# Kernel tuning notes

Measured on AMD Instinct MI355X. Metric: run time of the kernel, lower is better.

Reference implementation:

```python
import jax, jax.numpy as jnp
import numpy as np

N, E, D = 20000, 320000, 256
H, C = 8, 32  # heads, per-head channels (out_channels // heads)


def setup_inputs() -> dict:
    key = jax.random.key(0)
    ks = jax.random.split(key, 12)
    s = 1.0 / np.sqrt(D)
    return {
        "x": jax.random.normal(ks[0], (N, D), jnp.float32),
        "edge_index": jax.random.randint(ks[1], (2, E), 0, N, jnp.int64),
        "edge_attr": jax.random.normal(ks[2], (E, D), jnp.float32),
        "Wq": jax.random.normal(ks[3], (D, H * C), jnp.float32) * s,
        "bq": jnp.zeros((H * C,), jnp.float32),
        "Wk": jax.random.normal(ks[4], (D, H * C), jnp.float32) * s,
        "bk": jnp.zeros((H * C,), jnp.float32),
        "Wv": jax.random.normal(ks[5], (D, H * C), jnp.float32) * s,
        "bv": jnp.zeros((H * C,), jnp.float32),
        "We": jax.random.normal(ks[6], (D, H * C), jnp.float32) * s,  # lin_edge, no bias
        "Ws": jax.random.normal(ks[7], (D, H * C), jnp.float32) * s,  # lin_skip (root weight)
        "bs": jnp.zeros((H * C,), jnp.float32),
    }


def reference(x, edge_index, edge_attr, Wq, bq, Wk, bk, Wv, bv, We, Ws, bs):
    n = x.shape[0]
    src, dst = edge_index[0], edge_index[1]  # j (source), i (target)
    q = (x @ Wq + bq).reshape(n, H, C)
    k = (x @ Wk + bk).reshape(n, H, C)
    v = (x @ Wv + bv).reshape(n, H, C)
    e = (edge_attr @ We).reshape(-1, H, C)  # (E, H, C)

    kj = k[src] + e                      # key of source node + edge embedding
    alpha = jnp.einsum('ehc,ehc->eh', q[dst], kj) / jnp.sqrt(jnp.float32(C))
    # numerically-stable segment softmax over destination neighborhoods
    amax = jax.ops.segment_max(alpha, dst, num_segments=n)      # (N, H)
    ea = jnp.exp(alpha - amax[dst])                             # (E, H)
    denom = jax.ops.segment_sum(ea, dst, num_segments=n)        # (N, H)
    alpha = ea / (denom[dst] + 1e-16)

    msg = (v[src] + e) * alpha[:, :, None]                      # (E, H, C)
    out = jax.ops.segment_sum(msg, dst, num_segments=n)         # (N, H, C)
    out = out.reshape(n, H * C) + (x @ Ws + bs)                 # concat heads + skip
    return out
```

## Files before the change

### kernel.cpp

```cpp
#include <hip/hip_runtime.h>
#include <hip/hip_fp16.h>

#define N_NODES 20000
#define N_EDGES 320000
#define DIM 256

typedef _Float16 f16;
typedef unsigned int u32;
typedef f16 f16x8 __attribute__((ext_vector_type(8)));
typedef f16 f16x4 __attribute__((ext_vector_type(4)));
typedef float f32x4 __attribute__((ext_vector_type(4)));

#define GLL16(gsrc, ldst) __builtin_amdgcn_global_load_lds( \
    (const u32 __attribute__((address_space(1)))*)(gsrc),   \
    (u32 __attribute__((address_space(3)))*)(ldst), 16, 0, 0)

__global__ void prep_all(const float* __restrict__ Wq, const float* __restrict__ Wk,
                         const float* __restrict__ Wv, const float* __restrict__ Ws,
                         const float* __restrict__ We,
                         const float* __restrict__ bq, const float* __restrict__ bk,
                         const float* __restrict__ bv, const float* __restrict__ bs,
                         f16* __restrict__ wtbase, float* __restrict__ biasAll,
                         int* __restrict__ deg) {
    if (blockIdx.x < 1280) {
        int gid = blockIdx.x * 256 + threadIdx.x;
        int w = gid >> 16;
        int idx = gid & 65535;
        int k = idx >> 8, n = idx & 255;
        const float* W = (w == 0) ? Wq : (w == 1) ? Wk : (w == 2) ? Wv : (w == 3) ? Ws : We;
        wtbase[w * 65536 + n * 256 + k] = (f16)W[k * 256 + n];
    } else if (blockIdx.x < 1284) {
        int i = (blockIdx.x - 1280) * 256 + threadIdx.x;
        int y = i >> 8, col = i & 255;
        const float* b = (y == 0) ? bq : (y == 1) ? bk : (y == 2) ? bv : bs;
        biasAll[i] = b[col];
    } else {
        int i = (blockIdx.x - 1284) * 256 + threadIdx.x;
        if (i < N_NODES) deg[i] = 0;
    }
}

template<int EDGE>
__global__ __launch_bounds__(512, 4) void gemm_v4(
    const float* __restrict__ A, const f16* __restrict__ WTbase,
    const float* __restrict__ biasAll, const int* __restrict__ eids,
    f16* __restrict__ outF16, float* __restrict__ outF32, int M)
{
    __shared__ __align__(16) char lds[65536];
    const int tid = threadIdx.x;
    const int wave = tid >> 6, lane = tid & 63;
    const int l16 = lane & 15, lg = lane >> 4;
    const int y = blockIdx.y;
    const int outSel  = EDGE ? 4 : (y >> 1);
    const int colHalf = EDGE ? y : (y & 1);
    const f16* __restrict__ WT = WTbase + outSel * 65536 + colHalf * 128 * 256;
    const int rowBase = blockIdx.x * 128 + wave * 16;

    const int slot = rowBase + l16;
    int arow;
    if (EDGE) arow = eids[slot];
    else      arow = (slot < M) ? slot : M - 1;
    const float* ap = A + (size_t)arow * DIM;
    f32x4 lo[8], hi[8];
#pragma unroll
    for (int ks = 0; ks < 8; ++ks) {
        lo[ks] = *(const f32x4*)(ap + ks * 32 + lg * 8);
        hi[ks] = *(const f32x4*)(ap + ks * 32 + lg * 8 + 4);
    }

    {
        const int p = lane & 31;
#pragma unroll
        for (int r = 0; r < 8; ++r) {
            const int nrel = wave * 16 + r * 2 + (lane >> 5);
            const f16* src = WT + nrel * 256 + (p ^ (nrel & 31)) * 8;
            GLL16(src, &lds[(wave * 16 + r * 2) * 512]);
        }
    }

    f16x8 afr[8];
#pragma unroll
    for (int ks = 0; ks < 8; ++ks) {
#pragma unroll
        for (int j = 0; j < 4; ++j) {
            afr[ks][j]     = (f16)lo[ks][j];
            afr[ks][4 + j] = (f16)hi[ks][j];
        }
    }

    f32x4 acc[8];
#pragma unroll
    for (int c = 0; c < 8; ++c) acc[c] = (f32x4){0.f, 0.f, 0.f, 0.f};

    __syncthreads();

#pragma unroll
    for (int ks = 0; ks < 8; ++ks) {
#pragma unroll
        for (int ct = 0; ct < 8; ++ct) {
            const int nrel = ct * 16 + l16;
            f16x8 b = *(const f16x8*)(lds + nrel * 512 + (((ks * 4 + lg) ^ (nrel & 31)) * 16));
            acc[ct] = __builtin_amdgcn_mfma_f32_16x16x32_f16(afr[ks], b, acc[ct], 0, 0, 0);
        }
    }

#pragma unroll
    for (int ct = 0; ct < 8; ++ct) {
        const int col = colHalf * 128 + ct * 16 + l16;
        const float bv = EDGE ? 0.f : biasAll[outSel * 256 + col];
#pragma unroll
        for (int i = 0; i < 4; ++i) {
            const int row = rowBase + lg * 4 + i;
            if (EDGE || row < M) {
                const float val = acc[ct][i] + bv;
                if (EDGE) {
                    outF16[(size_t)row * 256 + col] = (f16)val;
                } else if (outSel < 3) {
                    (outF16 + (size_t)outSel * N_NODES * 256)[(size_t)row * 256 + col] = (f16)val;
                } else {
                    outF32[(size_t)row * 256 + col] = val;
                }
            }
        }
    }
}

__global__ void count_deg(const int* __restrict__ dst, int* __restrict__ deg) {
    int e = blockIdx.x * blockDim.x + threadIdx.x;
    if (e < N_EDGES) atomicAdd(&deg[dst[e]], 1);
}

__global__ __launch_bounds__(1024) void scan_deg(const int* __restrict__ deg,
                                                 int* __restrict__ rowptr,
                                                 int* __restrict__ cursor) {
    __shared__ int part[1024];
    const int t = threadIdx.x;
    const int CH = (N_NODES + 1023) / 1024;
    const int base = t * CH;
    int s = 0;
    for (int i = 0; i < CH; ++i) { int n = base + i; if (n < N_NODES) s += deg[n]; }
    part[t] = s;
    __syncthreads();
    for (int off = 1; off < 1024; off <<= 1) {
        int v = (t >= off) ? part[t - off] : 0;
        __syncthreads();
        part[t] += v;
        __syncthreads();
    }
    int run = (t == 0) ? 0 : part[t - 1];
    for (int i = 0; i < CH; ++i) {
        int n = base + i;
        if (n < N_NODES) { int dn = deg[n]; rowptr[n] = run; cursor[n] = run; run += dn; }
    }
    if (t == 1023) rowptr[N_NODES] = part[1023];
}

__global__ void scatter_edges(const int* __restrict__ src, const int* __restrict__ dst,
                              int* __restrict__ cursor,
                              int* __restrict__ eids, int* __restrict__ srcs) {
    int e = blockIdx.x * blockDim.x + threadIdx.x;
    if (e < N_EDGES) {
        int p = atomicAdd(&cursor[dst[e]], 1);
        eids[p] = e;
        srcs[p] = src[e];
    }
}

__global__ __launch_bounds__(256) void aggregate(
    const f16* __restrict__ qf, const f16* __restrict__ kf, const f16* __restrict__ vf,
    const f16* __restrict__ ef, const int* __restrict__ srcs,
    const int* __restrict__ rowptr, float* __restrict__ out)
{
    const int wave = threadIdx.x >> 6;
    const int lane = threadIdx.x & 63;
    const int node = blockIdx.x * 4 + wave;
    if (node >= N_NODES) return;
    const int c0 = lane * 4;

    f32x4 qv;
    {
        f16x4 qh = *(const f16x4*)(qf + (size_t)node * 256 + c0);
        qv = (f32x4){(float)qh[0], (float)qh[1], (float)qh[2], (float)qh[3]};
    }
    float acc0 = 0.f, acc1 = 0.f, acc2 = 0.f, acc3 = 0.f, den = 0.f;
    const int beg = rowptr[node], end = rowptr[node + 1];

#define BODY(ii) {                                                              \
        const int src = srcs[ii];                                               \
        f16x4 eh = *(const f16x4*)(ef + (size_t)(ii) * 256 + c0);               \
        f16x4 kh = *(const f16x4*)(kf + (size_t)src * 256 + c0);                \
        f16x4 vh = *(const f16x4*)(vf + (size_t)src * 256 + c0);                \
        const float e0 = (float)eh[0], e1 = (float)eh[1];                       \
        const float e2 = (float)eh[2], e3 = (float)eh[3];                       \
        float d = qv[0] * ((float)kh[0] + e0) + qv[1] * ((float)kh[1] + e1)     \
                + qv[2] * ((float)kh[2] + e2) + qv[3] * ((float)kh[3] + e3);    \
        d += __shfl_xor(d, 1);                                                  \
        d += __shfl_xor(d, 2);                                                  \
        d += __shfl_xor(d, 4);                                                  \
        const float w_ = __expf(d * 0.1767766952966369f);                       \
        den += w_;                                                              \
        acc0 += w_ * ((float)vh[0] + e0);                                       \
        acc1 += w_ * ((float)vh[1] + e1);                                       \
        acc2 += w_ * ((float)vh[2] + e2);                                       \
        acc3 += w_ * ((float)vh[3] + e3);                                       \
    }

    int idx = beg;
    for (; idx + 1 < end; idx += 2) { BODY(idx); BODY(idx + 1); }
    if (idx < end) BODY(idx);
#undef BODY

    const float inv = 1.0f / (den + 1e-16f);
    const size_t ob = (size_t)node * 256 + c0;
    f32x4 o = *(f32x4*)(out + ob);
    o[0] += acc0 * inv; o[1] += acc1 * inv; o[2] += acc2 * inv; o[3] += acc3 * inv;
    *(f32x4*)(out + ob) = o;
}

extern "C" void kernel_launch(void* const* d_in, const int* in_sizes, int n_in,
                              void* d_out, int out_size, void* d_ws, size_t ws_size,
                              hipStream_t stream) {
    const float* x   = (const float*)d_in[0];
    const int*   ei  = (const int*)d_in[1];
    const float* ea  = (const float*)d_in[2];
    const float* Wq  = (const float*)d_in[3];
    const float* bq  = (const float*)d_in[4];
    const float* Wk  = (const float*)d_in[5];
    const float* bk  = (const float*)d_in[6];
    const float* Wv  = (const float*)d_in[7];
    const float* bv  = (const float*)d_in[8];
    const float* We  = (const float*)d_in[9];
    const float* Ws  = (const float*)d_in[10];
    const float* bs  = (const float*)d_in[11];
    float* out = (float*)d_out;

    const int* srcArr = ei;
    const int* dstArr = ei + N_EDGES;

    char* w = (char*)d_ws;
    size_t off = 0;
    f16* wtbase = (f16*)(w + off); off += 5 * 65536 * 2;
    f16* qf = (f16*)(w + off); off += (size_t)N_NODES * 256 * 2;
    f16* kf = (f16*)(w + off); off += (size_t)N_NODES * 256 * 2;
    f16* vf = (f16*)(w + off); off += (size_t)N_NODES * 256 * 2;
    f16* ef = (f16*)(w + off); off += (size_t)N_EDGES * 256 * 2;
    int* deg    = (int*)(w + off); off += 80016;
    int* rowptr = (int*)(w + off); off += 80016;
    int* cursor = (int*)(w + off); off += 80016;
    int* eids   = (int*)(w + off); off += (size_t)N_EDGES * 4;
    int* srcs   = (int*)(w + off); off += (size_t)N_EDGES * 4;
    float* biasAll = (float*)(w + off); off += 4 * 256 * 4;
    (void)ws_size; (void)n_in; (void)in_sizes; (void)out_size;

    prep_all<<<1284 + (N_NODES + 255) / 256, 256, 0, stream>>>(
        Wq, Wk, Wv, Ws, We, bq, bk, bv, bs, wtbase, biasAll, deg);

    count_deg<<<(N_EDGES + 255) / 256, 256, 0, stream>>>(dstArr, deg);
    scan_deg<<<1, 1024, 0, stream>>>(deg, rowptr, cursor);
    scatter_edges<<<(N_EDGES + 255) / 256, 256, 0, stream>>>(srcArr, dstArr, cursor, eids, srcs);

    dim3 gnode((N_NODES + 127) / 128, 8);
    gemm_v4<0><<<gnode, 512, 0, stream>>>(x, wtbase, biasAll, nullptr, qf, out, N_NODES);
    dim3 gedge(N_EDGES / 128, 2);
    gemm_v4<1><<<gedge, 512, 0, stream>>>(ea, wtbase, nullptr, eids, ef, nullptr, N_EDGES);

    aggregate<<<N_NODES / 4, 256, 0, stream>>>(qf, kf, vf, ef, srcs, rowptr, out);
}
```

Baseline: 389.6 us.

## Make GEMMs persistent with software-pipelined A loads, scatter edge outputs, unroll aggregate

Both projection GEMMs become persistent kernels with a fixed grid of 512 blocks. Each block loads its weight slice into LDS once and loops over row tiles, prefetching the next half-tile of A while the MFMAs run. The edge GEMM now reads edge_attr contiguously and scatters results into CSR order through a slot-of-edge map, instead of gathering rows through eids. The aggregate loop is unrolled by 4 with all loads issued up front to raise memory-level parallelism, at the cost of more registers and scattered f16 writes.

```diff
diff --git a/kernel.cpp b/kernel.cpp
--- a/kernel.cpp
+++ b/kernel.cpp
@@ -41,32 +41,26 @@
 }
 
 template<int EDGE>
-__global__ __launch_bounds__(512, 4) void gemm_v4(
+__global__ __launch_bounds__(512, 4) void gemm_v5(
     const float* __restrict__ A, const f16* __restrict__ WTbase,
-    const float* __restrict__ biasAll, const int* __restrict__ eids,
-    f16* __restrict__ outF16, float* __restrict__ outF32, int M)
+    const float* __restrict__ biasAll, const int* __restrict__ slotOf,
+    f16* __restrict__ outF16, float* __restrict__ outF32)
 {
     __shared__ __align__(16) char lds[65536];
     const int tid = threadIdx.x;
     const int wave = tid >> 6, lane = tid & 63;
     const int l16 = lane & 15, lg = lane >> 4;
-    const int y = blockIdx.y;
-    const int outSel  = EDGE ? 4 : (y >> 1);
-    const int colHalf = EDGE ? y : (y & 1);
-    const f16* __restrict__ WT = WTbase + outSel * 65536 + colHalf * 128 * 256;
-    const int rowBase = blockIdx.x * 128 + wave * 16;
-
-    const int slot = rowBase + l16;
-    int arow;
-    if (EDGE) arow = eids[slot];
-    else      arow = (slot < M) ? slot : M - 1;
-    const float* ap = A + (size_t)arow * DIM;
-    f32x4 lo[8], hi[8];
-#pragma unroll
-    for (int ks = 0; ks < 8; ++ks) {
-        lo[ks] = *(const f32x4*)(ap + ks * 32 + lg * 8);
-        hi[ks] = *(const f32x4*)(ap + ks * 32 + lg * 8 + 4);
-    }
+
+    int outSel, colHalf, x, xStride, tilesX, M;
+    if (EDGE) {
+        outSel = 4; colHalf = blockIdx.x & 1;
+        x = blockIdx.x >> 1; xStride = 256; tilesX = N_EDGES / 128; M = N_EDGES;
+    } else {
+        const int y = blockIdx.x >> 6;
+        outSel = y >> 1; colHalf = y & 1;
+        x = blockIdx.x & 63; xStride = 64; tilesX = (N_NODES + 127) / 128; M = N_NODES;
+    }
+    const f16* __restrict__ WT = WTbase + outSel * 65536 + colHalf * (128 * 256);
 
     {
         const int p = lane & 31;
@@ -78,51 +72,113 @@
         }
     }
 
-    f16x8 afr[8];
-#pragma unroll
-    for (int ks = 0; ks < 8; ++ks) {
-#pragma unroll
-        for (int j = 0; j < 4; ++j) {
-            afr[ks][j]     = (f16)lo[ks][j];
-            afr[ks][4 + j] = (f16)hi[ks][j];
-        }
-    }
-
-    f32x4 acc[8];
-#pragma unroll
-    for (int c = 0; c < 8; ++c) acc[c] = (f32x4){0.f, 0.f, 0.f, 0.f};
+    float bias_[8];
+    if (!EDGE) {
+#pragma unroll
+        for (int ct = 0; ct < 8; ++ct)
+            bias_[ct] = biasAll[outSel * 256 + colHalf * 128 + ct * 16 + l16];
+    }
 
     __syncthreads();
 
-#pragma unroll
-    for (int ks = 0; ks < 8; ++ks) {
+    f32x4 lo[4], hi[4];
+
+#define ISSUE_A(ap_, h_) do {                                                  \
+    _Pragma("unroll")                                                          \
+    for (int ks_ = 0; ks_ < 4; ++ks_) {                                        \
+        lo[ks_] = *(const f32x4*)((ap_) + (h_) * 128 + ks_ * 32 + lg * 8);     \
+        hi[ks_] = *(const f32x4*)((ap_) + (h_) * 128 + ks_ * 32 + lg * 8 + 4); \
+    } } while (0)
+
+    int row0 = x * 128 + wave * 16 + l16;
+    if (!EDGE && row0 >= M) row0 = M - 1;
+    const float* apCur = A + (size_t)row0 * DIM;
+    ISSUE_A(apCur, 0);
+
+    for (; x < tilesX; x += xStride) {
+        const int rowBase = x * 128;
+        f32x4 acc[8];
+#pragma unroll
+        for (int c = 0; c < 8; ++c) acc[c] = (f32x4){0.f, 0.f, 0.f, 0.f};
+
+        f16x8 afr0[4];
+#pragma unroll
+        for (int ks = 0; ks < 4; ++ks) {
+#pragma unroll
+            for (int j = 0; j < 4; ++j) {
+                afr0[ks][j]     = (f16)lo[ks][j];
+                afr0[ks][4 + j] = (f16)hi[ks][j];
+            }
+        }
+        ISSUE_A(apCur, 1);
+
+        int srow[4];
+        if (EDGE) {
+#pragma unroll
+            for (int i = 0; i < 4; ++i)
+                srow[i] = slotOf[rowBase + wave * 16 + lg * 4 + i];
+        }
+
+#pragma unroll
+        for (int ks = 0; ks < 4; ++ks) {
+#pragma unroll
+            for (int ct = 0; ct < 8; ++ct) {
+                const int nrel = ct * 16 + l16;
+                const int kc = ks * 4 + lg;
+                f16x8 b = *(const f16x8*)(lds + nrel * 512 + ((kc ^ (nrel & 31)) * 16));
+                acc[ct] = __builtin_amdgcn_mfma_f32_16x16x32_f16(afr0[ks], b, acc[ct], 0, 0, 0);
+            }
+        }
+
+        f16x8 afr1[4];
+#pragma unroll
+        for (int ks = 0; ks < 4; ++ks) {
+#pragma unroll
+            for (int j = 0; j < 4; ++j) {
+                afr1[ks][j]     = (f16)lo[ks][j];
+                afr1[ks][4 + j] = (f16)hi[ks][j];
+            }
+        }
+        {
+            const int xn = x + xStride;
+            int rowN = (xn < tilesX) ? (xn * 128 + wave * 16 + l16) : row0;
+            if (!EDGE && rowN >= M) rowN = M - 1;
+            const float* apNext = A + (size_t)rowN * DIM;
+            ISSUE_A(apNext, 0);
+            apCur = apNext;
+            row0 = rowN;
+        }
+
+#pragma unroll
+        for (int ks = 0; ks < 4; ++ks) {
+#pragma unroll
+            for (int ct = 0; ct < 8; ++ct) {
+                const int nrel = ct * 16 + l16;
+                const int kc = 16 + ks * 4 + lg;
+                f16x8 b = *(const f16x8*)(lds + nrel * 512 + ((kc ^ (nrel & 31)) * 16));
+                acc[ct] = __builtin_amdgcn_mfma_f32_16x16x32_f16(afr1[ks], b, acc[ct], 0, 0, 0);
+            }
+        }
+
 #pragma unroll
         for (int ct = 0; ct < 8; ++ct) {
-            const int nrel = ct * 16 + l16;
-            f16x8 b = *(const f16x8*)(lds + nrel * 512 + (((ks * 4 + lg) ^ (nrel & 31)) * 16));
-            acc[ct] = __builtin_amdgcn_mfma_f32_16x16x32_f16(afr[ks], b, acc[ct], 0, 0, 0);
-        }
-    }
-
-#pragma unroll
-    for (int ct = 0; ct < 8; ++ct) {
-        const int col = colHalf * 128 + ct * 16 + l16;
-        const float bv = EDGE ? 0.f : biasAll[outSel * 256 + col];
-#pragma unroll
-        for (int i = 0; i < 4; ++i) {
-            const int row = rowBase + lg * 4 + i;
-            if (EDGE || row < M) {
-                const float val = acc[ct][i] + bv;
+            const int col = colHalf * 128 + ct * 16 + l16;
+#pragma unroll
+            for (int i = 0; i < 4; ++i) {
+                const int row = rowBase + wave * 16 + lg * 4 + i;
                 if (EDGE) {
-                    outF16[(size_t)row * 256 + col] = (f16)val;
-                } else if (outSel < 3) {
-                    (outF16 + (size_t)outSel * N_NODES * 256)[(size_t)row * 256 + col] = (f16)val;
-                } else {
-                    outF32[(size_t)row * 256 + col] = val;
+                    outF16[(size_t)srow[i] * 256 + col] = (f16)acc[ct][i];
+                } else if (row < M) {
+                    const float val = acc[ct][i] + bias_[ct];
+                    if (outSel < 3)
+                        (outF16 + (size_t)outSel * N_NODES * 256)[(size_t)row * 256 + col] = (f16)val;
+                    else
+                        outF32[(size_t)row * 256 + col] = val;
                 }
             }
         }
     }
+#undef ISSUE_A
 }
 
 __global__ void count_deg(const int* __restrict__ dst, int* __restrict__ deg) {
@@ -157,11 +213,11 @@
 
 __global__ void scatter_edges(const int* __restrict__ src, const int* __restrict__ dst,
                               int* __restrict__ cursor,
-                              int* __restrict__ eids, int* __restrict__ srcs) {
+                              int* __restrict__ slotOf, int* __restrict__ srcs) {
     int e = blockIdx.x * blockDim.x + threadIdx.x;
     if (e < N_EDGES) {
         int p = atomicAdd(&cursor[dst[e]], 1);
-        eids[p] = e;
+        slotOf[e] = p;
         srcs[p] = src[e];
     }
 }
@@ -185,29 +241,46 @@
     float acc0 = 0.f, acc1 = 0.f, acc2 = 0.f, acc3 = 0.f, den = 0.f;
     const int beg = rowptr[node], end = rowptr[node + 1];
 
-#define BODY(ii) {                                                              \
-        const int src = srcs[ii];                                               \
-        f16x4 eh = *(const f16x4*)(ef + (size_t)(ii) * 256 + c0);               \
-        f16x4 kh = *(const f16x4*)(kf + (size_t)src * 256 + c0);                \
-        f16x4 vh = *(const f16x4*)(vf + (size_t)src * 256 + c0);                \
-        const float e0 = (float)eh[0], e1 = (float)eh[1];                       \
-        const float e2 = (float)eh[2], e3 = (float)eh[3];                       \
-        float d = qv[0] * ((float)kh[0] + e0) + qv[1] * ((float)kh[1] + e1)     \
-                + qv[2] * ((float)kh[2] + e2) + qv[3] * ((float)kh[3] + e3);    \
-        d += __shfl_xor(d, 1);                                                  \
-        d += __shfl_xor(d, 2);                                                  \
-        d += __shfl_xor(d, 4);                                                  \
-        const float w_ = __expf(d * 0.1767766952966369f);                       \
-        den += w_;                                                              \
-        acc0 += w_ * ((float)vh[0] + e0);                                       \
-        acc1 += w_ * ((float)vh[1] + e1);                                       \
-        acc2 += w_ * ((float)vh[2] + e2);                                       \
-        acc3 += w_ * ((float)vh[3] + e3);                                       \
+#define BODY(eh, kh, vh) {                                                      \
+        const float _e0 = (float)(eh)[0], _e1 = (float)(eh)[1];                 \
+        const float _e2 = (float)(eh)[2], _e3 = (float)(eh)[3];                 \
+        float _d = qv[0] * ((float)(kh)[0] + _e0) + qv[1] * ((float)(kh)[1] + _e1) \
+                 + qv[2] * ((float)(kh)[2] + _e2) + qv[3] * ((float)(kh)[3] + _e3); \
+        _d += __shfl_xor(_d, 1);                                                \
+        _d += __shfl_xor(_d, 2);                                                \
+        _d += __shfl_xor(_d, 4);                                                \
+        const float _w = __expf(_d * 0.1767766952966369f);                      \
+        den += _w;                                                              \
+        acc0 += _w * ((float)(vh)[0] + _e0);                                    \
+        acc1 += _w * ((float)(vh)[1] + _e1);                                    \
+        acc2 += _w * ((float)(vh)[2] + _e2);                                    \
+        acc3 += _w * ((float)(vh)[3] + _e3);                                    \
     }
 
     int idx = beg;
-    for (; idx + 1 < end; idx += 2) { BODY(idx); BODY(idx + 1); }
-    if (idx < end) BODY(idx);
+    for (; idx + 4 <= end; idx += 4) {
+        const int s0 = srcs[idx], s1 = srcs[idx + 1], s2 = srcs[idx + 2], s3 = srcs[idx + 3];
+        f16x4 ea0 = *(const f16x4*)(ef + (size_t)(idx + 0) * 256 + c0);
+        f16x4 ea1 = *(const f16x4*)(ef + (size_t)(idx + 1) * 256 + c0);
+        f16x4 ea2 = *(const f16x4*)(ef + (size_t)(idx + 2) * 256 + c0);
+        f16x4 ea3 = *(const f16x4*)(ef + (size_t)(idx + 3) * 256 + c0);
+        f16x4 ka0 = *(const f16x4*)(kf + (size_t)s0 * 256 + c0);
+        f16x4 ka1 = *(const f16x4*)(kf + (size_t)s1 * 256 + c0);
+        f16x4 ka2 = *(const f16x4*)(kf + (size_t)s2 * 256 + c0);
+        f16x4 ka3 = *(const f16x4*)(kf + (size_t)s3 * 256 + c0);
+        f16x4 va0 = *(const f16x4*)(vf + (size_t)s0 * 256 + c0);
+        f16x4 va1 = *(const f16x4*)(vf + (size_t)s1 * 256 + c0);
+        f16x4 va2 = *(const f16x4*)(vf + (size_t)s2 * 256 + c0);
+        f16x4 va3 = *(const f16x4*)(vf + (size_t)s3 * 256 + c0);
+        BODY(ea0, ka0, va0); BODY(ea1, ka1, va1); BODY(ea2, ka2, va2); BODY(ea3, ka3, va3);
+    }
+    for (; idx < end; ++idx) {
+        const int s = srcs[idx];
+        f16x4 eh1 = *(const f16x4*)(ef + (size_t)idx * 256 + c0);
+        f16x4 kh1 = *(const f16x4*)(kf + (size_t)s * 256 + c0);
+        f16x4 vh1 = *(const f16x4*)(vf + (size_t)s * 256 + c0);
+        BODY(eh1, kh1, vh1);
+    }
 #undef BODY
 
     const float inv = 1.0f / (den + 1e-16f);
@@ -247,7 +320,7 @@
     int* deg    = (int*)(w + off); off += 80016;
     int* rowptr = (int*)(w + off); off += 80016;
     int* cursor = (int*)(w + off); off += 80016;
-    int* eids   = (int*)(w + off); off += (size_t)N_EDGES * 4;
+    int* slotOf = (int*)(w + off); off += (size_t)N_EDGES * 4;
     int* srcs   = (int*)(w + off); off += (size_t)N_EDGES * 4;
     float* biasAll = (float*)(w + off); off += 4 * 256 * 4;
     (void)ws_size; (void)n_in; (void)in_sizes; (void)out_size;
@@ -257,12 +330,10 @@
 
     count_deg<<<(N_EDGES + 255) / 256, 256, 0, stream>>>(dstArr, deg);
     scan_deg<<<1, 1024, 0, stream>>>(deg, rowptr, cursor);
-    scatter_edges<<<(N_EDGES + 255) / 256, 256, 0, stream>>>(srcArr, dstArr, cursor, eids, srcs);
-
-    dim3 gnode((N_NODES + 127) / 128, 8);
-    gemm_v4<0><<<gnode, 512, 0, stream>>>(x, wtbase, biasAll, nullptr, qf, out, N_NODES);
-    dim3 gedge(N_EDGES / 128, 2);
-    gemm_v4<1><<<gedge, 512, 0, stream>>>(ea, wtbase, nullptr, eids, ef, nullptr, N_EDGES);
+    scatter_edges<<<(N_EDGES + 255) / 256, 256, 0, stream>>>(srcArr, dstArr, cursor, slotOf, srcs);
+
+    gemm_v5<0><<<512, 512, 0, stream>>>(x, wtbase, biasAll, nullptr, qf, out);
+    gemm_v5<1><<<512, 512, 0, stream>>>(ea, wtbase, nullptr, slotOf, ef, nullptr);
 
     aggregate<<<N_NODES / 4, 256, 0, stream>>>(qf, kf, vf, ef, srcs, rowptr, out);
 }
```

Measured after the change: 863.9 us. 2.22x slower.

## Replace per-edge edge-projection GEMM with per-node query-folded projections

Applied to the files above, without the earlier changes.

The per-edge GEMM that projected edge_attr through We for all 320k edges is removed. Each node's query is instead pre-multiplied by We per head (G = q·We_h^T), so attention logits read raw fp32 edge_attr and dot it with G. Alpha-weighted raw edge features are accumulated per node and projected through We afterwards by a small node-level GEMM. This cuts the edge GEMM work and the fp16 edge buffer write and read, but the aggregation now streams 1KB of fp32 edge_attr per edge instead of 512B of fp16, and it adds per-node 8x256 state and two extra kernels.

```diff
diff --git a/kernel.cpp b/kernel.cpp
--- a/kernel.cpp
+++ b/kernel.cpp
@@ -20,8 +20,8 @@
                          const float* __restrict__ We,
                          const float* __restrict__ bq, const float* __restrict__ bk,
                          const float* __restrict__ bv, const float* __restrict__ bs,
-                         f16* __restrict__ wtbase, float* __restrict__ biasAll,
-                         int* __restrict__ deg) {
+                         f16* __restrict__ wtbase, f16* __restrict__ wef16,
+                         float* __restrict__ biasAll, int* __restrict__ deg) {
     if (blockIdx.x < 1280) {
         int gid = blockIdx.x * 256 + threadIdx.x;
         int w = gid >> 16;
@@ -29,37 +29,36 @@
         int k = idx >> 8, n = idx & 255;
         const float* W = (w == 0) ? Wq : (w == 1) ? Wk : (w == 2) ? Wv : (w == 3) ? Ws : We;
         wtbase[w * 65536 + n * 256 + k] = (f16)W[k * 256 + n];
-    } else if (blockIdx.x < 1284) {
-        int i = (blockIdx.x - 1280) * 256 + threadIdx.x;
+    } else if (blockIdx.x < 1536) {
+        int idx = (blockIdx.x - 1280) * 256 + threadIdx.x;
+        wef16[idx] = (f16)We[idx];
+    } else if (blockIdx.x < 1540) {
+        int i = (blockIdx.x - 1536) * 256 + threadIdx.x;
         int y = i >> 8, col = i & 255;
         const float* b = (y == 0) ? bq : (y == 1) ? bk : (y == 2) ? bv : bs;
         biasAll[i] = b[col];
     } else {
-        int i = (blockIdx.x - 1284) * 256 + threadIdx.x;
+        int i = (blockIdx.x - 1540) * 256 + threadIdx.x;
         if (i < N_NODES) deg[i] = 0;
     }
 }
 
-template<int EDGE>
-__global__ __launch_bounds__(512, 4) void gemm_v4(
+__global__ __launch_bounds__(512, 4) void gemm_qkvs(
     const float* __restrict__ A, const f16* __restrict__ WTbase,
-    const float* __restrict__ biasAll, const int* __restrict__ eids,
-    f16* __restrict__ outF16, float* __restrict__ outF32, int M)
+    const float* __restrict__ biasAll,
+    f16* __restrict__ outF16, float* __restrict__ outF32)
 {
     __shared__ __align__(16) char lds[65536];
     const int tid = threadIdx.x;
     const int wave = tid >> 6, lane = tid & 63;
     const int l16 = lane & 15, lg = lane >> 4;
     const int y = blockIdx.y;
-    const int outSel  = EDGE ? 4 : (y >> 1);
-    const int colHalf = EDGE ? y : (y & 1);
+    const int outSel = y >> 1, colHalf = y & 1;
     const f16* __restrict__ WT = WTbase + outSel * 65536 + colHalf * 128 * 256;
     const int rowBase = blockIdx.x * 128 + wave * 16;
 
     const int slot = rowBase + l16;
-    int arow;
-    if (EDGE) arow = eids[slot];
-    else      arow = (slot < M) ? slot : M - 1;
+    const int arow = (slot < N_NODES) ? slot : N_NODES - 1;
     const float* ap = A + (size_t)arow * DIM;
     f32x4 lo[8], hi[8];
 #pragma unroll
@@ -67,7 +66,6 @@
         lo[ks] = *(const f32x4*)(ap + ks * 32 + lg * 8);
         hi[ks] = *(const f32x4*)(ap + ks * 32 + lg * 8 + 4);
     }
-
     {
         const int p = lane & 31;
 #pragma unroll
@@ -77,7 +75,6 @@
             GLL16(src, &lds[(wave * 16 + r * 2) * 512]);
         }
     }
-
     f16x8 afr[8];
 #pragma unroll
     for (int ks = 0; ks < 8; ++ks) {
@@ -87,7 +84,6 @@
             afr[ks][4 + j] = (f16)hi[ks][j];
         }
     }
-
     f32x4 acc[8];
 #pragma unroll
     for (int c = 0; c < 8; ++c) acc[c] = (f32x4){0.f, 0.f, 0.f, 0.f};
@@ -103,24 +99,53 @@
             acc[ct] = __builtin_amdgcn_mfma_f32_16x16x32_f16(afr[ks], b, acc[ct], 0, 0, 0);
         }
     }
-
 #pragma unroll
     for (int ct = 0; ct < 8; ++ct) {
         const int col = colHalf * 128 + ct * 16 + l16;
-        const float bv = EDGE ? 0.f : biasAll[outSel * 256 + col];
+        const float bv = biasAll[outSel * 256 + col];
 #pragma unroll
         for (int i = 0; i < 4; ++i) {
             const int row = rowBase + lg * 4 + i;
-            if (EDGE || row < M) {
+            if (row < N_NODES) {
                 const float val = acc[ct][i] + bv;
-                if (EDGE) {
-                    outF16[(size_t)row * 256 + col] = (f16)val;
-                } else if (outSel < 3) {
+                if (outSel < 3)
                     (outF16 + (size_t)outSel * N_NODES * 256)[(size_t)row * 256 + col] = (f16)val;
-                } else {
+                else
                     outF32[(size_t)row * 256 + col] = val;
-                }
             }
+        }
+    }
+}
+
+__global__ __launch_bounds__(256, 4) void gemm_g(
+    const f16* __restrict__ qf, const f16* __restrict__ wef16, f16* __restrict__ G)
+{
+    const int tid = threadIdx.x;
+    const int wave = tid >> 6, lane = tid & 63;
+    const int l16 = lane & 15, lg = lane >> 4;
+    const int h = blockIdx.y;
+    const int rowBase = blockIdx.x * 64 + wave * 16;
+
+    int arow = rowBase + l16;
+    if (arow >= N_NODES) arow = N_NODES - 1;
+    f16x8 a = *(const f16x8*)(qf + (size_t)arow * 256 + h * 32 + lg * 8);
+
+    f32x4 acc[16];
+#pragma unroll
+    for (int c = 0; c < 16; ++c) acc[c] = (f32x4){0.f, 0.f, 0.f, 0.f};
+#pragma unroll
+    for (int ct = 0; ct < 16; ++ct) {
+        f16x8 b = *(const f16x8*)(wef16 + (size_t)(ct * 16 + l16) * 256 + h * 32 + lg * 8);
+        acc[ct] = __builtin_amdgcn_mfma_f32_16x16x32_f16(a, b, acc[ct], 0, 0, 0);
+    }
+#pragma unroll
+    for (int ct = 0; ct < 16; ++ct) {
+        const int d = ct * 16 + l16;
+#pragma unroll
+        for (int i = 0; i < 4; ++i) {
+            const int row = rowBase + lg * 4 + i;
+            if (row < N_NODES)
+                G[(size_t)row * 2048 + h * 256 + d] = (f16)acc[ct][i];
         }
     }
 }
@@ -166,15 +191,17 @@
     }
 }
 
-__global__ __launch_bounds__(256) void aggregate(
+__global__ __launch_bounds__(256) void aggregate3(
     const f16* __restrict__ qf, const f16* __restrict__ kf, const f16* __restrict__ vf,
-    const f16* __restrict__ ef, const int* __restrict__ srcs,
+    f16* __restrict__ G, const float* __restrict__ ea,
+    const int* __restrict__ eids, const int* __restrict__ srcs,
     const int* __restrict__ rowptr, float* __restrict__ out)
 {
     const int wave = threadIdx.x >> 6;
     const int lane = threadIdx.x & 63;
     const int node = blockIdx.x * 4 + wave;
     if (node >= N_NODES) return;
+    const int h = lane >> 3, j = lane & 7;
     const int c0 = lane * 4;
 
     f32x4 qv;
@@ -182,39 +209,106 @@
         f16x4 qh = *(const f16x4*)(qf + (size_t)node * 256 + c0);
         qv = (f32x4){(float)qh[0], (float)qh[1], (float)qh[2], (float)qh[3]};
     }
-    float acc0 = 0.f, acc1 = 0.f, acc2 = 0.f, acc3 = 0.f, den = 0.f;
+    f32x4 ga[8];
+#pragma unroll
+    for (int m = 0; m < 8; ++m) {
+        f16x4 gh = *(const f16x4*)(G + (size_t)node * 2048 + h * 256 + m * 32 + j * 4);
+        ga[m] = (f32x4){(float)gh[0], (float)gh[1], (float)gh[2], (float)gh[3]};
+    }
+
+    f32x4 z[8];
+#pragma unroll
+    for (int m = 0; m < 8; ++m) z[m] = (f32x4){0.f, 0.f, 0.f, 0.f};
+    f32x4 va = (f32x4){0.f, 0.f, 0.f, 0.f};
+    float den = 0.f;
     const int beg = rowptr[node], end = rowptr[node + 1];
 
-#define BODY(ii) {                                                              \
-        const int src = srcs[ii];                                               \
-        f16x4 eh = *(const f16x4*)(ef + (size_t)(ii) * 256 + c0);               \
-        f16x4 kh = *(const f16x4*)(kf + (size_t)src * 256 + c0);                \
-        f16x4 vh = *(const f16x4*)(vf + (size_t)src * 256 + c0);                \
-        const float e0 = (float)eh[0], e1 = (float)eh[1];                       \
-        const float e2 = (float)eh[2], e3 = (float)eh[3];                       \
-        float d = qv[0] * ((float)kh[0] + e0) + qv[1] * ((float)kh[1] + e1)     \
-                + qv[2] * ((float)kh[2] + e2) + qv[3] * ((float)kh[3] + e3);    \
-        d += __shfl_xor(d, 1);                                                  \
-        d += __shfl_xor(d, 2);                                                  \
-        d += __shfl_xor(d, 4);                                                  \
-        const float w_ = __expf(d * 0.1767766952966369f);                       \
-        den += w_;                                                              \
-        acc0 += w_ * ((float)vh[0] + e0);                                       \
-        acc1 += w_ * ((float)vh[1] + e1);                                       \
-        acc2 += w_ * ((float)vh[2] + e2);                                       \
-        acc3 += w_ * ((float)vh[3] + e3);                                       \
-    }
-
-    int idx = beg;
-    for (; idx + 1 < end; idx += 2) { BODY(idx); BODY(idx + 1); }
-    if (idx < end) BODY(idx);
-#undef BODY
+    int eid = 0, src = 0;
+    if (beg < end) { eid = eids[beg]; src = srcs[beg]; }
+    for (int idx = beg; idx < end; ++idx) {
+        const int eidN = (idx + 1 < end) ? eids[idx + 1] : 0;
+        const int srcN = (idx + 1 < end) ? srcs[idx + 1] : 0;
+        const float* ep = ea + (size_t)eid * 256 + j * 4;
+        f32x4 e0 = *(const f32x4*)(ep + 0 * 32);
+        f32x4 e1 = *(const f32x4*)(ep + 1 * 32);
+        f32x4 e2 = *(const f32x4*)(ep + 2 * 32);
+        f32x4 e3 = *(const f32x4*)(ep + 3 * 32);
+        f32x4 e4 = *(const f32x4*)(ep + 4 * 32);
+        f32x4 e5 = *(const f32x4*)(ep + 5 * 32);
+        f32x4 e6 = *(const f32x4*)(ep + 6 * 32);
+        f32x4 e7 = *(const f32x4*)(ep + 7 * 32);
+        f16x4 kh = *(const f16x4*)(kf + (size_t)src * 256 + c0);
+        f16x4 vh = *(const f16x4*)(vf + (size_t)src * 256 + c0);
+
+        float p = 0.f;
+#define DOT4(ev, m_) p += (ev)[0]*ga[m_][0] + (ev)[1]*ga[m_][1] + (ev)[2]*ga[m_][2] + (ev)[3]*ga[m_][3]
+        DOT4(e0, 0); DOT4(e1, 1); DOT4(e2, 2); DOT4(e3, 3);
+        DOT4(e4, 4); DOT4(e5, 5); DOT4(e6, 6); DOT4(e7, 7);
+#undef DOT4
+        p += qv[0]*(float)kh[0] + qv[1]*(float)kh[1] + qv[2]*(float)kh[2] + qv[3]*(float)kh[3];
+        p += __shfl_xor(p, 1);
+        p += __shfl_xor(p, 2);
+        p += __shfl_xor(p, 4);
+        const float al = __expf(p * 0.1767766952966369f);
+        den += al;
+        va[0] += al * (float)vh[0]; va[1] += al * (float)vh[1];
+        va[2] += al * (float)vh[2]; va[3] += al * (float)vh[3];
+#define ZACC(ev, m_) { z[m_][0] += al*(ev)[0]; z[m_][1] += al*(ev)[1]; z[m_][2] += al*(ev)[2]; z[m_][3] += al*(ev)[3]; }
+        ZACC(e0, 0); ZACC(e1, 1); ZACC(e2, 2); ZACC(e3, 3);
+        ZACC(e4, 4); ZACC(e5, 5); ZACC(e6, 6); ZACC(e7, 7);
+#undef ZACC
+        eid = eidN; src = srcN;
+    }
 
     const float inv = 1.0f / (den + 1e-16f);
     const size_t ob = (size_t)node * 256 + c0;
     f32x4 o = *(f32x4*)(out + ob);
-    o[0] += acc0 * inv; o[1] += acc1 * inv; o[2] += acc2 * inv; o[3] += acc3 * inv;
+    o[0] += va[0] * inv; o[1] += va[1] * inv; o[2] += va[2] * inv; o[3] += va[3] * inv;
     *(f32x4*)(out + ob) = o;
+#pragma unroll
+    for (int m = 0; m < 8; ++m) {
+        f16x4 zh;
+        zh[0] = (f16)(z[m][0] * inv); zh[1] = (f16)(z[m][1] * inv);
+        zh[2] = (f16)(z[m][2] * inv); zh[3] = (f16)(z[m][3] * inv);
+        *(f16x4*)(G + (size_t)node * 2048 + h * 256 + m * 32 + j * 4) = zh;
+    }
+}
+
+__global__ __launch_bounds__(512, 4) void gemm_z2(
+    const f16* __restrict__ zf, const f16* __restrict__ WTe, float* __restrict__ out)
+{
+    const int tid = threadIdx.x;
+    const int wave = tid >> 6, lane = tid & 63;
+    const int l16 = lane & 15, lg = lane >> 4;
+    const int h = blockIdx.y;
+    const int rowBase = blockIdx.x * 128 + wave * 16;
+
+    int arow = rowBase + l16;
+    if (arow >= N_NODES) arow = N_NODES - 1;
+    const f16* ap = zf + (size_t)arow * 2048 + h * 256 + lg * 8;
+
+    f32x4 acc[2];
+    acc[0] = (f32x4){0.f, 0.f, 0.f, 0.f};
+    acc[1] = (f32x4){0.f, 0.f, 0.f, 0.f};
+#pragma unroll
+    for (int ks = 0; ks < 8; ++ks) {
+        f16x8 a = *(const f16x8*)(ap + ks * 32);
+#pragma unroll
+        for (int ct = 0; ct < 2; ++ct) {
+            f16x8 b = *(const f16x8*)(WTe + (size_t)(h * 32 + ct * 16 + l16) * 256 + ks * 32 + lg * 8);
+            acc[ct] = __builtin_amdgcn_mfma_f32_16x16x32_f16(a, b, acc[ct], 0, 0, 0);
+        }
+    }
+#pragma unroll
+    for (int ct = 0; ct < 2; ++ct) {
+        const int col = h * 32 + ct * 16 + l16;
+#pragma unroll
+        for (int i = 0; i < 4; ++i) {
+            const int row = rowBase + lg * 4 + i;
+            if (row < N_NODES)
+                out[(size_t)row * 256 + col] += acc[ct][i];
+        }
+    }
 }
 
 extern "C" void kernel_launch(void* const* d_in, const int* in_sizes, int n_in,
@@ -240,10 +334,11 @@
     char* w = (char*)d_ws;
     size_t off = 0;
     f16* wtbase = (f16*)(w + off); off += 5 * 65536 * 2;
+    f16* wef16  = (f16*)(w + off); off += 65536 * 2;
     f16* qf = (f16*)(w + off); off += (size_t)N_NODES * 256 * 2;
     f16* kf = (f16*)(w + off); off += (size_t)N_NODES * 256 * 2;
     f16* vf = (f16*)(w + off); off += (size_t)N_NODES * 256 * 2;
-    f16* ef = (f16*)(w + off); off += (size_t)N_EDGES * 256 * 2;
+    f16* G  = (f16*)(w + off); off += (size_t)N_NODES * 2048 * 2;
     int* deg    = (int*)(w + off); off += 80016;
     int* rowptr = (int*)(w + off); off += 80016;
     int* cursor = (int*)(w + off); off += 80016;
@@ -252,17 +347,22 @@
     float* biasAll = (float*)(w + off); off += 4 * 256 * 4;
     (void)ws_size; (void)n_in; (void)in_sizes; (void)out_size;
 
-    prep_all<<<1284 + (N_NODES + 255) / 256, 256, 0, stream>>>(
-        Wq, Wk, Wv, Ws, We, bq, bk, bv, bs, wtbase, biasAll, deg);
+    prep_all<<<1540 + (N_NODES + 255) / 256, 256, 0, stream>>>(
+        Wq, Wk, Wv, Ws, We, bq, bk, bv, bs, wtbase, wef16, biasAll, deg);
 
     count_deg<<<(N_EDGES + 255) / 256, 256, 0, stream>>>(dstArr, deg);
     scan_deg<<<1, 1024, 0, stream>>>(deg, rowptr, cursor);
     scatter_edges<<<(N_EDGES + 255) / 256, 256, 0, stream>>>(srcArr, dstArr, cursor, eids, srcs);
 
     dim3 gnode((N_NODES + 127) / 128, 8);
-    gemm_v4<0><<<gnode, 512, 0, stream>>>(x, wtbase, biasAll, nullptr, qf, out, N_NODES);
-    dim3 gedge(N_EDGES / 128, 2);
-    gemm_v4<1><<<gedge, 512, 0, stream>>>(ea, wtbase, nullptr, eids, ef, nullptr, N_EDGES);
-
-    aggregate<<<N_NODES / 4, 256, 0, stream>>>(qf, kf, vf, ef, srcs, rowptr, out);
-}
+    gemm_qkvs<<<gnode, 512, 0, stream>>>(x, wtbase, biasAll, qf, out);
+
+    dim3 gg((N_NODES + 63) / 64, 8);
+    gemm_g<<<gg, 256, 0, stream>>>(qf, wef16, G);
+
+    aggregate3<<<(N_NODES + 3) / 4, 256, 0, stream>>>(
+        qf, kf, vf, G, ea, eids, srcs, rowptr, out);
+
+    dim3 gz((N_NODES + 127) / 128, 8);
+    gemm_z2<<<gz, 512, 0, stream>>>(G, wtbase + 4 * 65536, out);
+}
```

Measured after the change: 449.7 us. +15.4%, slower.
